# Optimization experiments

Hardware: AMD Instinct MI355X
Metric: run time of the kernel (lower is better)

The kernel has to match this reference:

```python
import jax, jax.numpy as jnp
import numpy as np

B, T, F, H, P, HEADS = 1024, 128, 9, 256, 2048, 4
DH = H // HEADS

def _lstm_layer(x, Wih, Whh, bih, bhh):
    # x: [B,T,in]; gate order i,f,g,o (torch convention)
    xp = jnp.einsum('bti,gi->btg', x, Wih) + bih + bhh  # [B,T,4H]
    h0 = jnp.zeros((x.shape[0], Whh.shape[1]), x.dtype)
    def step(carry, xt):
        h, c = carry
        g = xt + h @ Whh.T
        i, f, gg, o = jnp.split(g, 4, axis=-1)
        c = jax.nn.sigmoid(f) * c + jax.nn.sigmoid(i) * jnp.tanh(gg)
        h = jax.nn.sigmoid(o) * jnp.tanh(c)
        return (h, c), h
    _, hs = jax.lax.scan(step, (h0, h0), jnp.swapaxes(xp, 0, 1))
    return jnp.swapaxes(hs, 0, 1)  # [B,T,H]

def _layernorm(x, g, b, eps=1e-5):
    mu = x.mean(-1, keepdims=True)
    var = ((x - mu) ** 2).mean(-1, keepdims=True)
    return (x - mu) * jax.lax.rsqrt(var + eps) * g + b

def setup_inputs():
    key = jax.random.key(0)
    ks = jax.random.split(key, 30)
    w = lambda k, s: jax.random.normal(k, s, jnp.float32) * 0.05
    return {
        'x': jax.random.normal(ks[0], (B, T, F), jnp.float32),
        'sku_indices': jnp.arange(B, dtype=jnp.int32),
        'adj': jax.random.uniform(ks[1], (P, P), jnp.float32),
        'vsn_emb_w': w(ks[2], (F, H)), 'vsn_emb_b': w(ks[3], (F, H)),
        'vsn_sel_w': w(ks[4], (F, F)), 'vsn_sel_b': w(ks[5], (F,)),
        'lstm_Wih0': w(ks[6], (4 * H, H)), 'lstm_Whh0': w(ks[7], (4 * H, H)),
        'lstm_bih0': w(ks[8], (4 * H,)), 'lstm_bhh0': w(ks[9], (4 * H,)),
        'lstm_Wih1': w(ks[10], (4 * H, H)), 'lstm_Whh1': w(ks[11], (4 * H, H)),
        'lstm_bih1': w(ks[12], (4 * H,)), 'lstm_bhh1': w(ks[13], (4 * H,)),
        'attn_in_w': w(ks[14], (3 * H, H)), 'attn_in_b': w(ks[15], (3 * H,)),
        'attn_out_w': w(ks[16], (H, H)), 'attn_out_b': w(ks[17], (H,)),
        'gnn_w': w(ks[18], (H, H)), 'gnn_b': w(ks[19], (H,)),
        'ln_g': jnp.ones((H,), jnp.float32), 'ln_b': jnp.zeros((H,), jnp.float32),
        'gate_w': w(ks[20], (H, 2 * H)), 'gate_b': w(ks[21], (H,)),
        'out_w': w(ks[22], (1, H)), 'out_b': w(ks[23], (1,)),
    }

def reference(x, sku_indices, adj, vsn_emb_w, vsn_emb_b, vsn_sel_w, vsn_sel_b,
              lstm_Wih0, lstm_Whh0, lstm_bih0, lstm_bhh0,
              lstm_Wih1, lstm_Whh1, lstm_bih1, lstm_bhh1,
              attn_in_w, attn_in_b, attn_out_w, attn_out_b,
              gnn_w, gnn_b, ln_g, ln_b, gate_w, gate_b, out_w, out_b):
    # --- TFT hidden: variable selection -> 2-layer LSTM -> MHA, take last step ---
    emb = x[..., None] * vsn_emb_w + vsn_emb_b           # [B,T,F,H]
    wts = jax.nn.softmax(x @ vsn_sel_w.T + vsn_sel_b, -1)  # [B,T,F]
    h = jnp.einsum('btf,btfh->bth', wts, emb)            # [B,T,H]
    h = _lstm_layer(h, lstm_Wih0, lstm_Whh0, lstm_bih0, lstm_bhh0)
    h = _lstm_layer(h, lstm_Wih1, lstm_Whh1, lstm_bih1, lstm_bhh1)
    qkv = h @ attn_in_w.T + attn_in_b                    # [B,T,3H]
    q, k, v = [a.reshape(B, T, HEADS, DH) for a in jnp.split(qkv, 3, axis=-1)]
    scores = jnp.einsum('bqhd,bkhd->bhqk', q, k) / np.sqrt(DH).astype(np.float32)
    attn = jax.nn.softmax(scores, -1)
    o = jnp.einsum('bhqk,bkhd->bqhd', attn, v).reshape(B, T, H)
    o = o @ attn_out_w.T + attn_out_b
    hidden = o[:, -1, :]                                  # [B,H]
    # --- GNN enrichment (all sku_indices valid here) ---
    product_embeds = jnp.zeros((P, H), hidden.dtype).at[sku_indices].set(hidden)
    degree = jnp.clip(adj.sum(1, keepdims=True), 1e-6)
    aggregated = (adj / degree) @ product_embeds          # [P,H]
    transformed = jax.nn.gelu(aggregated @ gnn_w.T + gnn_b, approximate=False)
    transformed = _layernorm(transformed, ln_g, ln_b)
    enriched = transformed[sku_indices]                   # [B,H]
    gate = jax.nn.sigmoid(jnp.concatenate([hidden, enriched], -1) @ gate_w.T + gate_b)
    combined = gate * enriched + (1.0 - gate) * hidden
    out = combined @ out_w.T + out_b                      # [B,1]
    return out.squeeze(-1)
```

## Files before the change

### kernel.cpp

```cpp
#include <hip/hip_runtime.h>
#include <hip/hip_fp16.h>

typedef _Float16 f16;
typedef _Float16 f16x8 __attribute__((ext_vector_type(8)));
typedef _Float16 f16x4 __attribute__((ext_vector_type(4)));
typedef float f32x4 __attribute__((ext_vector_type(4)));

#define B_ 1024
#define T_ 128
#define F_ 9
#define H_ 256
#define P_ 2048

typedef unsigned long long ull;
#define AL(p) __hip_atomic_load((p), __ATOMIC_RELAXED, __HIP_MEMORY_SCOPE_AGENT)
#define AS(p, v) __hip_atomic_store((p), (v), __ATOMIC_RELAXED, __HIP_MEMORY_SCOPE_AGENT)

__device__ __forceinline__ float sigf(float x) { return 1.f / (1.f + __expf(-x)); }
__device__ __forceinline__ float tanh_(float x) {
  float a = fminf(fabsf(x), 12.f);
  float e = __expf(2.f * a);
  float r = 1.f - 2.f / (e + 1.f);
  return copysignf(r, x);
}

__device__ __forceinline__ f16x8 aload16(const f16* p) {
  union { ull u[2]; f16x8 v; } r;
  r.u[0] = AL((const ull*)p);
  r.u[1] = AL((const ull*)p + 1);
  return r.v;
}

__device__ __forceinline__ float blk_sum(float v) {
  __shared__ float sh[8];
  int lane = threadIdx.x & 63, w = threadIdx.x >> 6;
  int nw = blockDim.x >> 6;
#pragma unroll
  for (int o = 32; o > 0; o >>= 1) v += __shfl_xor(v, o, 64);
  __syncthreads();
  if (lane == 0) sh[w] = v;
  __syncthreads();
  float t = 0.f;
  for (int i = 0; i < nw; i++) t += sh[i];
  return t;
}

__global__ __launch_bounds__(256) void gemm64(
    const f16* __restrict__ A, int lda,
    const f16* __restrict__ Bt, int ldb,
    const float* __restrict__ bias,
    f16* __restrict__ o16, int ldo16,
    float* __restrict__ o32, int ldo32,
    f16* __restrict__ o16t, int ldt,
    int M, int N, int K)
{
  __shared__ __align__(16) f16 As[64][40];
  __shared__ __align__(16) f16 Bs[64][40];
  const int tid = threadIdx.x;
  const int lane = tid & 63, wave = tid >> 6;
  const int q = lane >> 4, l15 = lane & 15;
  const int bm = blockIdx.x * 64, bn = blockIdx.y * 64;

  f32x4 acc[4];
#pragma unroll
  for (int tn = 0; tn < 4; tn++) acc[tn] = (f32x4){0.f, 0.f, 0.f, 0.f};

  for (int k0 = 0; k0 < K; k0 += 32) {
    int row = tid >> 2, kh = (tid & 3) * 8;
    *(f16x8*)&As[row][kh] = *(const f16x8*)&A[(size_t)(bm + row) * lda + k0 + kh];
    *(f16x8*)&Bs[row][kh] = *(const f16x8*)&Bt[(size_t)(bn + row) * ldb + k0 + kh];
    __syncthreads();
    f16x8 af = *(const f16x8*)&As[wave * 16 + l15][q * 8];
#pragma unroll
    for (int tn = 0; tn < 4; tn++) {
      f16x8 bf = *(const f16x8*)&Bs[tn * 16 + l15][q * 8];
      acc[tn] = __builtin_amdgcn_mfma_f32_16x16x32_f16(af, bf, acc[tn], 0, 0, 0);
    }
    __syncthreads();
  }
#pragma unroll
  for (int tn = 0; tn < 4; tn++) {
    int colg = bn + tn * 16 + l15;
    float bv = bias ? bias[colg] : 0.f;
#pragma unroll
    for (int r = 0; r < 4; r++) {
      int rowg = bm + wave * 16 + q * 4 + r;
      float v = acc[tn][r] + bv;
      if (o32) o32[(size_t)rowg * ldo32 + colg] = v;
      if (o16) o16[(size_t)rowg * ldo16 + colg] = (f16)v;
      if (o16t) o16t[(size_t)colg * ldt + rowg] = (f16)v;
    }
  }
}

__global__ __launch_bounds__(256, 1) void lstm_pipe(
    f16* __restrict__ hio,
    const f16* __restrict__ wpk0, const f16* __restrict__ wpk1,
    const float* __restrict__ b0, const float* __restrict__ b1,
    int* __restrict__ cnt0, int* __restrict__ cnt1)
{
  __shared__ __align__(16) f16 apf[2][16][64][8];
  __shared__ __align__(16) f16 htile[32][64];
  const int tid = threadIdx.x;
  const int lane = tid & 63, w = tid >> 6;
  const int q = lane >> 4, l15 = lane & 15;
  const int layer = blockIdx.x >> 7;
  const int lbid = blockIdx.x & 127;
  const int grp = lbid & 31, s = lbid >> 5;
  const int m0 = grp * 32;
  const f16* wpk = layer ? wpk1 : wpk0;
  const float* bias = layer ? b1 : b0;
  int* myflags = (layer ? cnt1 : cnt0) + grp * 64;
  int* xflags  = cnt0 + grp * 64;

  const int own0 = ((w >> 1) == s);
  const int own1 = (((w + 4) >> 1) == s);
  const int offh = (w & 1) * 32;

  f16x8 bf[4][16];
  {
    const f16* wbase = wpk + (((size_t)(s * 4 + w) * 4) * 16) * 512 + lane * 8;
#pragma unroll
    for (int g = 0; g < 4; g++)
#pragma unroll
      for (int k = 0; k < 16; k++)
        bf[g][k] = *(const f16x8*)(wbase + (size_t)(g * 16 + k) * 512);
  }
  float bv[4];
#pragma unroll
  for (int g = 0; g < 4; g++) bv[g] = bias[g * 256 + s * 64 + w * 16 + l15];

  const int srow = lane & 15, scb = lane >> 4;
  size_t rb[2];
  rb[0] = ((size_t)(m0 + srow) * T_) * 256 + scb * 8;
  rb[1] = ((size_t)(m0 + 16 + srow) * T_) * 256 + scb * 8;

  const f16x8 zv = {(f16)0, (f16)0, (f16)0, (f16)0, (f16)0, (f16)0, (f16)0, (f16)0};

  if (layer) {
    if (tid == 0) {
      int it = 0;
      for (;;) {
        ull a = AL((ull*)xflags);
        ull b2 = AL((ull*)xflags + 1);
        if ((int)a >= 2 && (int)(a >> 32) >= 2 &&
            (int)b2 >= 2 && (int)(b2 >> 32) >= 2) break;
        __builtin_amdgcn_s_sleep(1);
        if (++it > (1 << 22)) break;
      }
    }
    __syncthreads();
  }
  f16x8 xr[2][2];
#pragma unroll
  for (int mt = 0; mt < 2; mt++) {
    if (layer) {
      xr[mt][0] = aload16(&hio[rb[mt] + (size_t)w * 32]);
      xr[mt][1] = aload16(&hio[rb[mt] + (size_t)(w + 4) * 32]);
    } else {
      xr[mt][0] = *(const f16x8*)&hio[rb[mt] + (size_t)w * 32];
      xr[mt][1] = *(const f16x8*)&hio[rb[mt] + (size_t)(w + 4) * 32];
    }
  }
  float cst[2][4] = {{0.f, 0.f, 0.f, 0.f}, {0.f, 0.f, 0.f, 0.f}};

  __syncthreads();
  if (tid == 0) AS(&myflags[s], 1);

  for (int t = 0; t < T_; ++t) {
    if (tid == 0) {
      const int needO = t + 1;
      int needX = 0;
      if (layer) { needX = t + 3; if (needX > T_ + 1) needX = T_ + 1; }
      int it = 0;
      for (;;) {
        ull a = AL((ull*)myflags);
        ull b2 = AL((ull*)myflags + 1);
        bool ok = (int)a >= needO && (int)(a >> 32) >= needO &&
                  (int)b2 >= needO && (int)(b2 >> 32) >= needO;
        if (ok && layer) {
          ull c = AL((ull*)xflags);
          ull d = AL((ull*)xflags + 1);
          ok = (int)c >= needX && (int)(c >> 32) >= needX &&
               (int)d >= needX && (int)(d >> 32) >= needX;
        }
        if (ok) break;
        __builtin_amdgcn_s_sleep(1);
        if (++it > (1 << 22)) break;
      }
    }
    __syncthreads();

#pragma unroll
    for (int mt = 0; mt < 2; mt++) {
      *(f16x8*)&apf[mt][w][lane][0]     = xr[mt][0];
      *(f16x8*)&apf[mt][w + 4][lane][0] = xr[mt][1];
      f16x8 h0 = zv, h1 = zv;
      if (t > 0) {
        if (own0) h0 = *(const f16x8*)&htile[mt * 16 + srow][offh + scb * 8];
        else      h0 = aload16(&hio[rb[mt] + (size_t)(t - 1) * 256 + (size_t)w * 32]);
        if (own1) h1 = *(const f16x8*)&htile[mt * 16 + srow][offh + scb * 8];
        else      h1 = aload16(&hio[rb[mt] + (size_t)(t - 1) * 256 + (size_t)(w + 4) * 32]);
      }
      *(f16x8*)&apf[mt][8 + w][lane][0]  = h0;
      *(f16x8*)&apf[mt][12 + w][lane][0] = h1;
    }
    __syncthreads();

    f32x4 acc[2][4];
#pragma unroll
    for (int mt = 0; mt < 2; mt++)
#pragma unroll
      for (int g = 0; g < 4; g++) acc[mt][g] = (f32x4){0.f, 0.f, 0.f, 0.f};
#pragma unroll
    for (int k = 0; k < 16; k++) {
      f16x8 a0 = *(const f16x8*)&apf[0][k][lane][0];
      f16x8 a1 = *(const f16x8*)&apf[1][k][lane][0];
#pragma unroll
      for (int g = 0; g < 4; g++) {
        acc[0][g] = __builtin_amdgcn_mfma_f32_16x16x32_f16(a0, bf[g][k], acc[0][g], 0, 0, 0);
        acc[1][g] = __builtin_amdgcn_mfma_f32_16x16x32_f16(a1, bf[g][k], acc[1][g], 0, 0, 0);
      }
    }
    if (t + 1 < T_) {
#pragma unroll
      for (int mt = 0; mt < 2; mt++) {
        if (layer) {
          xr[mt][0] = aload16(&hio[rb[mt] + (size_t)(t + 1) * 256 + (size_t)w * 32]);
          xr[mt][1] = aload16(&hio[rb[mt] + (size_t)(t + 1) * 256 + (size_t)(w + 4) * 32]);
        } else {
          xr[mt][0] = *(const f16x8*)&hio[rb[mt] + (size_t)(t + 1) * 256 + (size_t)w * 32];
          xr[mt][1] = *(const f16x8*)&hio[rb[mt] + (size_t)(t + 1) * 256 + (size_t)(w + 4) * 32];
        }
      }
    }
    f16 hn[2][4];
#pragma unroll
    for (int mt = 0; mt < 2; mt++)
#pragma unroll
      for (int r = 0; r < 4; r++) {
        float ip = acc[mt][0][r] + bv[0];
        float fp = acc[mt][1][r] + bv[1];
        float gp = acc[mt][2][r] + bv[2];
        float op = acc[mt][3][r] + bv[3];
        float cn = sigf(fp) * cst[mt][r] + sigf(ip) * tanh_(gp);
        cst[mt][r] = cn;
        hn[mt][r] = (f16)(sigf(op) * tanh_(cn));
      }
#pragma unroll
    for (int mt = 0; mt < 2; mt++)
#pragma unroll
      for (int r = 0; r < 4; r++)
        htile[mt * 16 + q * 4 + r][w * 16 + l15] = hn[mt][r];
    __syncthreads();
    {
      int row = tid >> 3, c8 = (tid & 7) * 8;
      union { ull u[2]; f16x8 v; } uh;
      uh.v = *(const f16x8*)&htile[row][c8];
      ull* dst =
          (ull*)&hio[((size_t)(m0 + row) * T_ + t) * 256 + s * 64 + c8];
      AS(dst, uh.u[0]);
      AS(dst + 1, uh.u[1]);
    }
    __syncthreads();
    if (tid == 0) AS(&myflags[s], t + 2);
  }
}

__global__ __launch_bounds__(256) void vsn_fused_kernel(
    const float* __restrict__ x, const float* __restrict__ selw,
    const float* __restrict__ selb, const float* __restrict__ embw,
    const float* __restrict__ embb, f16* __restrict__ hout)
{
  __shared__ float wbs[128][18];
  int b = blockIdx.x, tid = threadIdx.x;
  if (tid < 128) {
    size_t pos = (size_t)b * 128 + tid;
    const float* xr = x + pos * F_;
    float xv[F_];
#pragma unroll
    for (int f = 0; f < F_; f++) xv[f] = xr[f];
    float wv[F_]; float mx = -1e30f;
#pragma unroll
    for (int f = 0; f < F_; f++) {
      float s = selb[f];
#pragma unroll
      for (int f2 = 0; f2 < F_; f2++) s += xv[f2] * selw[f * F_ + f2];
      wv[f] = s; mx = fmaxf(mx, s);
    }
    float se = 0.f;
#pragma unroll
    for (int f = 0; f < F_; f++) { wv[f] = __expf(wv[f] - mx); se += wv[f]; }
    float inv = 1.f / se;
#pragma unroll
    for (int f = 0; f < F_; f++) {
      float wt = wv[f] * inv;
      wbs[tid][f] = wt; wbs[tid][9 + f] = wt * xv[f];
    }
  }
  __syncthreads();
  int j = tid;
  float ew[F_], eb[F_];
#pragma unroll
  for (int f = 0; f < F_; f++) { ew[f] = embw[f * H_ + j]; eb[f] = embb[f * H_ + j]; }
  for (int i = 0; i < 128; i++) {
    float h = 0.f;
#pragma unroll
    for (int f = 0; f < F_; f++) h += wbs[i][9 + f] * ew[f] + wbs[i][f] * eb[f];
    hout[((size_t)b * 128 + i) * H_ + j] = (f16)h;
  }
}

__global__ __launch_bounds__(256) void attn_fused_kernel(
    const f16* __restrict__ hseq, const float* __restrict__ qbuf,
    const float* __restrict__ attn_in_w, const float* __restrict__ attn_in_b,
    f16* __restrict__ aob)
{
  __shared__ __align__(16) f16 hs[T_][264];
  __shared__ float qs[256];
  __shared__ float qks[4][256];
  __shared__ float ps[4][T_];
  __shared__ float hb[4][256];
  int b = blockIdx.x, tid = threadIdx.x;
  for (int i = tid; i < T_ * 32; i += 256) {
    int row = i >> 5, cc = (i & 31) * 8;
    *(f16x8*)&hs[row][cc] = *(const f16x8*)&hseq[((size_t)b * T_ + row) * 256 + cc];
  }
  qs[tid] = qbuf[(size_t)b * 256 + tid];
  __syncthreads();
  {
    int j = tid;
#pragma unroll
    for (int h = 0; h < 4; h++) {
      float acc = 0.f;
      for (int d = 0; d < 64; d++)
        acc += qs[h * 64 + d] * attn_in_w[(size_t)(256 + h * 64 + d) * 256 + j];
      qks[h][j] = acc * 0.125f;
    }
  }
  __syncthreads();
  if (tid < T_) {
    float s[4] = {0.f, 0.f, 0.f, 0.f};
    for (int cc = 0; cc < 32; cc++) {
      f16x8 v = *(const f16x8*)&hs[tid][cc * 8];
#pragma unroll
      for (int h = 0; h < 4; h++) {
        float a = 0.f;
#pragma unroll
        for (int j = 0; j < 8; j++) a += qks[h][cc * 8 + j] * (float)v[j];
        s[h] += a;
      }
    }
#pragma unroll
    for (int h = 0; h < 4; h++) ps[h][tid] = s[h];
  }
  __syncthreads();
  {
    int w = tid >> 6, l = tid & 63;
    float a = ps[w][l], bb = ps[w][l + 64];
    float m = fmaxf(a, bb);
#pragma unroll
    for (int o = 32; o > 0; o >>= 1) m = fmaxf(m, __shfl_xor(m, o, 64));
    float e0 = __expf(a - m), e1 = __expf(bb - m);
    float se = e0 + e1;
#pragma unroll
    for (int o = 32; o > 0; o >>= 1) se += __shfl_xor(se, o, 64);
    float inv = 1.f / se;
    ps[w][l] = e0 * inv; ps[w][l + 64] = e1 * inv;
  }
  __syncthreads();
  {
    int j = tid;
    float acc[4] = {0.f, 0.f, 0.f, 0.f};
    for (int t = 0; t < T_; t++) {
      float hv = (float)hs[t][j];
#pragma unroll
      for (int h = 0; h < 4; h++) acc[h] += ps[h][t] * hv;
    }
#pragma unroll
    for (int h = 0; h < 4; h++) hb[h][j] = acc[h];
  }
  __syncthreads();
  {
    int d = tid, h = d >> 6;
    const float4* wr = (const float4*)(attn_in_w + (size_t)(512 + d) * 256);
    float acc = 0.f;
    for (int cc = 0; cc < 64; cc++) {
      float4 w4 = wr[cc];
      acc += w4.x * hb[h][cc * 4] + w4.y * hb[h][cc * 4 + 1]
           + w4.z * hb[h][cc * 4 + 2] + w4.w * hb[h][cc * 4 + 3];
    }
    aob[(size_t)b * 256 + d] = (f16)(acc + attn_in_b[512 + d]);
  }
}

__global__ __launch_bounds__(256) void gelu_ln_kernel(
    const float* __restrict__ pre, const float* __restrict__ lg,
    const float* __restrict__ lb, float* __restrict__ enr,
    f16* __restrict__ hidcat)
{
  int row = blockIdx.x, j = threadIdx.x;
  float xv = pre[row * 256 + j];
  float ge = 0.5f * xv * (1.f + erff(xv * 0.70710678118654752f));
  float mu = blk_sum(ge) * (1.f / 256.f);
  float d = ge - mu;
  float var = blk_sum(d * d) * (1.f / 256.f);
  float y = d * rsqrtf(var + 1e-5f) * lg[j] + lb[j];
  enr[row * 256 + j] = y;
  hidcat[row * 512 + 256 + j] = (f16)y;
}

__global__ __launch_bounds__(256) void final_kernel(
    const float* __restrict__ gpre, const float* __restrict__ enr,
    const float* __restrict__ hid, const float* __restrict__ outw,
    const float* __restrict__ outb, float* __restrict__ out)
{
  int b = blockIdx.x, j = threadIdx.x;
  float gt = sigf(gpre[b * 256 + j]);
  float comb = gt * enr[b * 256 + j] + (1.f - gt) * hid[b * 256 + j];
  float v = comb * outw[j];
  float s = blk_sum(v);
  if (j == 0) out[b] = s + outb[0];
}

__global__ void prep_kernel(
    const float* Wih0, const float* Whh0, const float* Wih1, const float* Whh1,
    const float* bih0, const float* bhh0, const float* bih1, const float* bhh1,
    const float* attn_in_w, const float* attn_out_w, const float* gnn_w,
    const float* gate_w, const float* adj, const int* sku,
    f16* wpk0, f16* wpk1, f16* attninf, f16* attnoutf, f16* gnnwf, f16* gatewf,
    float* bias0, float* bias1, int* flagz, f16* adjn)
{
  if (blockIdx.x >= 3353) {
    int bp = blockIdx.x - 3353;
    int p = sku[bp];
    int tid = threadIdx.x;
    float s = 0.f;
    for (int j = tid; j < P_; j += 256) s += adj[(size_t)p * P_ + j];
    float tot = blk_sum(s);
    float inv = 1.f / fmaxf(tot, 1e-6f);
    for (int b = tid; b < B_; b += 256)
      adjn[(size_t)bp * B_ + b] = (f16)(adj[(size_t)p * P_ + sku[b]] * inv);
    return;
  }
  int idx = blockIdx.x * 256 + threadIdx.x;
  if (idx < 524288) {
    int j = idx & 7, lane = (idx >> 3) & 63, k = (idx >> 9) & 15;
    int g = (idx >> 13) & 3, w = (idx >> 15) & 3, s = (idx >> 17) & 3;
    int row = g * 256 + s * 64 + w * 16 + (lane & 15);
    int col = k * 32 + (lane >> 4) * 8 + j;
    float v0 = col < 256 ? Wih0[(size_t)row * 256 + col] : Whh0[(size_t)row * 256 + col - 256];
    float v1 = col < 256 ? Wih1[(size_t)row * 256 + col] : Whh1[(size_t)row * 256 + col - 256];
    wpk0[idx] = (f16)v0;
    wpk1[idx] = (f16)v1;
    return;
  }
  int i = idx - 524288;
  if (i < 65536) { attninf[i] = (f16)attn_in_w[i]; return; }
  i -= 65536;
  if (i < 65536) { attnoutf[i] = (f16)attn_out_w[i]; return; }
  i -= 65536;
  if (i < 65536) { gnnwf[i] = (f16)gnn_w[i]; return; }
  i -= 65536;
  if (i < 131072) { gatewf[i] = (f16)gate_w[i]; return; }
  i -= 131072;
  if (i < 1024) { bias0[i] = bih0[i] + bhh0[i]; return; }
  i -= 1024;
  if (i < 1024) { bias1[i] = bih1[i] + bhh1[i]; return; }
  i -= 1024;
  if (i < 4096) { flagz[i] = 0; return; }
}

extern "C" void kernel_launch(void* const* d_in, const int* in_sizes, int n_in,
                              void* d_out, int out_size, void* d_ws, size_t ws_size,
                              hipStream_t stream)
{
  const float* x         = (const float*)d_in[0];
  const int*   sku       = (const int*)  d_in[1];
  const float* adj       = (const float*)d_in[2];
  const float* vsn_emb_w = (const float*)d_in[3];
  const float* vsn_emb_b = (const float*)d_in[4];
  const float* vsn_sel_w = (const float*)d_in[5];
  const float* vsn_sel_b = (const float*)d_in[6];
  const float* Wih0 = (const float*)d_in[7];
  const float* Whh0 = (const float*)d_in[8];
  const float* bih0 = (const float*)d_in[9];
  const float* bhh0 = (const float*)d_in[10];
  const float* Wih1 = (const float*)d_in[11];
  const float* Whh1 = (const float*)d_in[12];
  const float* bih1 = (const float*)d_in[13];
  const float* bhh1 = (const float*)d_in[14];
  const float* attn_in_w  = (const float*)d_in[15];
  const float* attn_in_b  = (const float*)d_in[16];
  const float* attn_out_w = (const float*)d_in[17];
  const float* attn_out_b = (const float*)d_in[18];
  const float* gnn_w  = (const float*)d_in[19];
  const float* gnn_b  = (const float*)d_in[20];
  const float* ln_g   = (const float*)d_in[21];
  const float* ln_b   = (const float*)d_in[22];
  const float* gate_w = (const float*)d_in[23];
  const float* gate_b = (const float*)d_in[24];
  const float* out_w  = (const float*)d_in[25];
  const float* out_b  = (const float*)d_in[26];
  (void)in_sizes; (void)n_in; (void)out_size; (void)ws_size;

  char* wsb = (char*)d_ws;
  size_t off = 0;
  auto alloc = [&](size_t bytes) -> void* {
    void* p = wsb + off;
    off += (bytes + 255) & ~(size_t)255;
    return p;
  };
  f16* hA      = (f16*)alloc((size_t)B_ * T_ * H_ * 2);
  f16* wpk0    = (f16*)alloc((size_t)1024 * 512 * 2);
  f16* wpk1    = (f16*)alloc((size_t)1024 * 512 * 2);
  f16* attninf = (f16*)alloc((size_t)256 * 256 * 2);
  f16* attnoutf= (f16*)alloc((size_t)256 * 256 * 2);
  f16* gnnwf   = (f16*)alloc((size_t)256 * 256 * 2);
  f16* gatewf  = (f16*)alloc((size_t)256 * 512 * 2);
  float* bias0 = (float*)alloc(1024 * 4);
  float* bias1 = (float*)alloc(1024 * 4);
  int* cnt0    = (int*)alloc(32 * 64 * 4);
  int* cnt1    = (int*)alloc(32 * 64 * 4);
  f16* adjn    = (f16*)alloc((size_t)B_ * B_ * 2);
  float* qbuf  = (float*)alloc((size_t)B_ * 256 * 4);
  f16* aob     = (f16*)alloc((size_t)B_ * 256 * 2);
  float* hidden32 = (float*)alloc((size_t)B_ * 256 * 4);
  f16* hidcat  = (f16*)alloc((size_t)B_ * 512 * 2);
  f16* hT      = (f16*)alloc((size_t)256 * B_ * 2);
  f16* aggf    = (f16*)alloc((size_t)B_ * 256 * 2);
  float* gnnpre= (float*)alloc((size_t)B_ * 256 * 4);
  float* enr32 = (float*)alloc((size_t)B_ * 256 * 4);
  float* gatepre=(float*)alloc((size_t)B_ * 256 * 4);

  prep_kernel<<<4377, 256, 0, stream>>>(
      Wih0, Whh0, Wih1, Whh1, bih0, bhh0, bih1, bhh1,
      attn_in_w, attn_out_w, gnn_w, gate_w, adj, sku,
      wpk0, wpk1, attninf, attnoutf, gnnwf, gatewf, bias0, bias1, cnt0, adjn);

  vsn_fused_kernel<<<B_, 256, 0, stream>>>(x, vsn_sel_w, vsn_sel_b,
                                           vsn_emb_w, vsn_emb_b, hA);
  lstm_pipe<<<256, 256, 0, stream>>>(hA, wpk0, wpk1, bias0, bias1, cnt0, cnt1);

  dim3 g64(B_ / 64, 256 / 64);
  gemm64<<<g64, 256, 0, stream>>>(hA + (size_t)(T_ - 1) * 256, T_ * 256, attninf, 256,
                                  attn_in_b, nullptr, 0, qbuf, 256, nullptr, 0,
                                  B_, 256, 256);
  attn_fused_kernel<<<B_, 256, 0, stream>>>(hA, qbuf, attn_in_w, attn_in_b, aob);
  gemm64<<<g64, 256, 0, stream>>>(aob, 256, attnoutf, 256, attn_out_b,
                                  hidcat, 512, hidden32, 256, hT, B_,
                                  B_, 256, 256);
  gemm64<<<g64, 256, 0, stream>>>(adjn, 1024, hT, 1024, nullptr,
                                  aggf, 256, nullptr, 0, nullptr, 0,
                                  B_, 256, 1024);
  gemm64<<<g64, 256, 0, stream>>>(aggf, 256, gnnwf, 256, gnn_b,
                                  nullptr, 0, gnnpre, 256, nullptr, 0,
                                  B_, 256, 256);
  gelu_ln_kernel<<<B_, 256, 0, stream>>>(gnnpre, ln_g, ln_b, enr32, hidcat);
  gemm64<<<g64, 256, 0, stream>>>(hidcat, 512, gatewf, 512, gate_b,
                                  nullptr, 0, gatepre, 256, nullptr, 0,
                                  B_, 256, 512);
  final_kernel<<<B_, 256, 0, stream>>>(gatepre, enr32, hidden32, out_w, out_b, (float*)d_out);
}
```

Baseline: 951.0 us.

## Fuse VSN into prep, q-projection into attention, and GNN/LN/gate tail into one kernel

```diff
diff --git a/kernel.cpp b/kernel.cpp
--- a/kernel.cpp
+++ b/kernel.cpp
@@ -267,52 +267,8 @@
   }
 }
 
-__global__ __launch_bounds__(256) void vsn_fused_kernel(
-    const float* __restrict__ x, const float* __restrict__ selw,
-    const float* __restrict__ selb, const float* __restrict__ embw,
-    const float* __restrict__ embb, f16* __restrict__ hout)
-{
-  __shared__ float wbs[128][18];
-  int b = blockIdx.x, tid = threadIdx.x;
-  if (tid < 128) {
-    size_t pos = (size_t)b * 128 + tid;
-    const float* xr = x + pos * F_;
-    float xv[F_];
-#pragma unroll
-    for (int f = 0; f < F_; f++) xv[f] = xr[f];
-    float wv[F_]; float mx = -1e30f;
-#pragma unroll
-    for (int f = 0; f < F_; f++) {
-      float s = selb[f];
-#pragma unroll
-      for (int f2 = 0; f2 < F_; f2++) s += xv[f2] * selw[f * F_ + f2];
-      wv[f] = s; mx = fmaxf(mx, s);
-    }
-    float se = 0.f;
-#pragma unroll
-    for (int f = 0; f < F_; f++) { wv[f] = __expf(wv[f] - mx); se += wv[f]; }
-    float inv = 1.f / se;
-#pragma unroll
-    for (int f = 0; f < F_; f++) {
-      float wt = wv[f] * inv;
-      wbs[tid][f] = wt; wbs[tid][9 + f] = wt * xv[f];
-    }
-  }
-  __syncthreads();
-  int j = tid;
-  float ew[F_], eb[F_];
-#pragma unroll
-  for (int f = 0; f < F_; f++) { ew[f] = embw[f * H_ + j]; eb[f] = embb[f * H_ + j]; }
-  for (int i = 0; i < 128; i++) {
-    float h = 0.f;
-#pragma unroll
-    for (int f = 0; f < F_; f++) h += wbs[i][9 + f] * ew[f] + wbs[i][f] * eb[f];
-    hout[((size_t)b * 128 + i) * H_ + j] = (f16)h;
-  }
-}
-
 __global__ __launch_bounds__(256) void attn_fused_kernel(
-    const f16* __restrict__ hseq, const float* __restrict__ qbuf,
+    const f16* __restrict__ hseq, const f16* __restrict__ attninf,
     const float* __restrict__ attn_in_w, const float* __restrict__ attn_in_b,
     f16* __restrict__ aob)
 {
@@ -326,7 +282,19 @@
     int row = i >> 5, cc = (i & 31) * 8;
     *(f16x8*)&hs[row][cc] = *(const f16x8*)&hseq[((size_t)b * T_ + row) * 256 + cc];
   }
-  qs[tid] = qbuf[(size_t)b * 256 + tid];
+  __syncthreads();
+  {
+    int j = tid;
+    float acc = attn_in_b[j];
+    const f16x8* wr = (const f16x8*)(attninf + (size_t)j * 256);
+    for (int cc = 0; cc < 32; cc++) {
+      f16x8 wv = wr[cc];
+      f16x8 hv = *(const f16x8*)&hs[T_ - 1][cc * 8];
+#pragma unroll
+      for (int u = 0; u < 8; u++) acc += (float)hv[u] * (float)wv[u];
+    }
+    qs[j] = acc;
+  }
   __syncthreads();
   {
     int j = tid;
@@ -394,30 +362,36 @@
   }
 }
 
-__global__ __launch_bounds__(256) void gelu_ln_kernel(
-    const float* __restrict__ pre, const float* __restrict__ lg,
-    const float* __restrict__ lb, float* __restrict__ enr,
-    f16* __restrict__ hidcat)
+__global__ __launch_bounds__(256) void tail_fused_kernel(
+    const f16* __restrict__ aggf, const f16* __restrict__ gnnwT,
+    const float* __restrict__ gnn_b, const float* __restrict__ lg,
+    const float* __restrict__ lb, const float* __restrict__ hid32,
+    const f16* __restrict__ gatewT, const float* __restrict__ gate_b,
+    const float* __restrict__ outw, const float* __restrict__ outb,
+    float* __restrict__ out)
 {
-  int row = blockIdx.x, j = threadIdx.x;
-  float xv = pre[row * 256 + j];
-  float ge = 0.5f * xv * (1.f + erff(xv * 0.70710678118654752f));
+  __shared__ float ag[256], yl[256], hl[256];
+  int b = blockIdx.x, j = threadIdx.x;
+  ag[j] = (float)aggf[(size_t)b * 256 + j];
+  hl[j] = hid32[(size_t)b * 256 + j];
+  __syncthreads();
+  float acc = gnn_b[j];
+#pragma unroll 8
+  for (int k = 0; k < 256; k++) acc += ag[k] * (float)gnnwT[k * 256 + j];
+  float ge = 0.5f * acc * (1.f + erff(acc * 0.70710678118654752f));
   float mu = blk_sum(ge) * (1.f / 256.f);
   float d = ge - mu;
   float var = blk_sum(d * d) * (1.f / 256.f);
   float y = d * rsqrtf(var + 1e-5f) * lg[j] + lb[j];
-  enr[row * 256 + j] = y;
-  hidcat[row * 512 + 256 + j] = (f16)y;
-}
-
-__global__ __launch_bounds__(256) void final_kernel(
-    const float* __restrict__ gpre, const float* __restrict__ enr,
-    const float* __restrict__ hid, const float* __restrict__ outw,
-    const float* __restrict__ outb, float* __restrict__ out)
-{
-  int b = blockIdx.x, j = threadIdx.x;
-  float gt = sigf(gpre[b * 256 + j]);
-  float comb = gt * enr[b * 256 + j] + (1.f - gt) * hid[b * 256 + j];
+  yl[j] = y;
+  __syncthreads();
+  float g = gate_b[j];
+#pragma unroll 8
+  for (int k = 0; k < 256; k++) g += hl[k] * (float)gatewT[k * 256 + j];
+#pragma unroll 8
+  for (int k = 0; k < 256; k++) g += yl[k] * (float)gatewT[(256 + k) * 256 + j];
+  float gt = sigf(g);
+  float comb = gt * y + (1.f - gt) * hl[j];
   float v = comb * outw[j];
   float s = blk_sum(v);
   if (j == 0) out[b] = s + outb[0];
@@ -428,9 +402,51 @@
     const float* bih0, const float* bhh0, const float* bih1, const float* bhh1,
     const float* attn_in_w, const float* attn_out_w, const float* gnn_w,
     const float* gate_w, const float* adj, const int* sku,
-    f16* wpk0, f16* wpk1, f16* attninf, f16* attnoutf, f16* gnnwf, f16* gatewf,
-    float* bias0, float* bias1, int* flagz, f16* adjn)
+    const float* x, const float* selw, const float* selb,
+    const float* embw, const float* embb,
+    f16* wpk0, f16* wpk1, f16* attninf, f16* attnoutf, f16* gnnwT, f16* gatewT,
+    float* bias0, float* bias1, int* flagz, f16* adjn, f16* hA)
 {
+  if (blockIdx.x >= 4377) {
+    __shared__ float wbs[128][18];
+    int b = blockIdx.x - 4377, tid = threadIdx.x;
+    if (tid < 128) {
+      size_t pos = (size_t)b * 128 + tid;
+      const float* xr = x + pos * F_;
+      float xv[F_];
+#pragma unroll
+      for (int f = 0; f < F_; f++) xv[f] = xr[f];
+      float wv[F_]; float mx = -1e30f;
+#pragma unroll
+      for (int f = 0; f < F_; f++) {
+        float s = selb[f];
+#pragma unroll
+        for (int f2 = 0; f2 < F_; f2++) s += xv[f2] * selw[f * F_ + f2];
+        wv[f] = s; mx = fmaxf(mx, s);
+      }
+      float se = 0.f;
+#pragma unroll
+      for (int f = 0; f < F_; f++) { wv[f] = __expf(wv[f] - mx); se += wv[f]; }
+      float inv = 1.f / se;
+#pragma unroll
+      for (int f = 0; f < F_; f++) {
+        float wt = wv[f] * inv;
+        wbs[tid][f] = wt; wbs[tid][9 + f] = wt * xv[f];
+      }
+    }
+    __syncthreads();
+    int j = threadIdx.x;
+    float ew[F_], eb[F_];
+#pragma unroll
+    for (int f = 0; f < F_; f++) { ew[f] = embw[f * H_ + j]; eb[f] = embb[f * H_ + j]; }
+    for (int i = 0; i < 128; i++) {
+      float h = 0.f;
+#pragma unroll
+      for (int f = 0; f < F_; f++) h += wbs[i][9 + f] * ew[f] + wbs[i][f] * eb[f];
+      hA[((size_t)b * 128 + i) * H_ + j] = (f16)h;
+    }
+    return;
+  }
   if (blockIdx.x >= 3353) {
     int bp = blockIdx.x - 3353;
     int p = sku[bp];
@@ -460,9 +476,17 @@
   i -= 65536;
   if (i < 65536) { attnoutf[i] = (f16)attn_out_w[i]; return; }
   i -= 65536;
-  if (i < 65536) { gnnwf[i] = (f16)gnn_w[i]; return; }
+  if (i < 65536) {
+    int j = i & 255, k = i >> 8;
+    gnnwT[i] = (f16)gnn_w[(size_t)j * 256 + k];
+    return;
+  }
   i -= 65536;
-  if (i < 131072) { gatewf[i] = (f16)gate_w[i]; return; }
+  if (i < 131072) {
+    int j = i & 255, k = i >> 8;
+    gatewT[i] = (f16)gate_w[(size_t)j * 512 + k];
+    return;
+  }
   i -= 131072;
   if (i < 1024) { bias0[i] = bih0[i] + bhh0[i]; return; }
   i -= 1024;
@@ -516,49 +540,35 @@
   f16* wpk1    = (f16*)alloc((size_t)1024 * 512 * 2);
   f16* attninf = (f16*)alloc((size_t)256 * 256 * 2);
   f16* attnoutf= (f16*)alloc((size_t)256 * 256 * 2);
-  f16* gnnwf   = (f16*)alloc((size_t)256 * 256 * 2);
-  f16* gatewf  = (f16*)alloc((size_t)256 * 512 * 2);
+  f16* gnnwT   = (f16*)alloc((size_t)256 * 256 * 2);
+  f16* gatewT  = (f16*)alloc((size_t)512 * 256 * 2);
   float* bias0 = (float*)alloc(1024 * 4);
   float* bias1 = (float*)alloc(1024 * 4);
   int* cnt0    = (int*)alloc(32 * 64 * 4);
   int* cnt1    = (int*)alloc(32 * 64 * 4);
   f16* adjn    = (f16*)alloc((size_t)B_ * B_ * 2);
-  float* qbuf  = (float*)alloc((size_t)B_ * 256 * 4);
   f16* aob     = (f16*)alloc((size_t)B_ * 256 * 2);
   float* hidden32 = (float*)alloc((size_t)B_ * 256 * 4);
-  f16* hidcat  = (f16*)alloc((size_t)B_ * 512 * 2);
   f16* hT      = (f16*)alloc((size_t)256 * B_ * 2);
   f16* aggf    = (f16*)alloc((size_t)B_ * 256 * 2);
-  float* gnnpre= (float*)alloc((size_t)B_ * 256 * 4);
-  float* enr32 = (float*)alloc((size_t)B_ * 256 * 4);
-  float* gatepre=(float*)alloc((size_t)B_ * 256 * 4);
-
-  prep_kernel<<<4377, 256, 0, stream>>>(
+
+  prep_kernel<<<5401, 256, 0, stream>>>(
       Wih0, Whh0, Wih1, Whh1, bih0, bhh0, bih1, bhh1,
       attn_in_w, attn_out_w, gnn_w, gate_w, adj, sku,
-      wpk0, wpk1, attninf, attnoutf, gnnwf, gatewf, bias0, bias1, cnt0, adjn);
-
-  vsn_fused_kernel<<<B_, 256, 0, stream>>>(x, vsn_sel_w, vsn_sel_b,
-                                           vsn_emb_w, vsn_emb_b, hA);
+      x, vsn_sel_w, vsn_sel_b, vsn_emb_w, vsn_emb_b,
+      wpk0, wpk1, attninf, attnoutf, gnnwT, gatewT, bias0, bias1, cnt0, adjn, hA);
+
   lstm_pipe<<<256, 256, 0, stream>>>(hA, wpk0, wpk1, bias0, bias1, cnt0, cnt1);
 
+  attn_fused_kernel<<<B_, 256, 0, stream>>>(hA, attninf, attn_in_w, attn_in_b, aob);
   dim3 g64(B_ / 64, 256 / 64);
-  gemm64<<<g64, 256, 0, stream>>>(hA + (size_t)(T_ - 1) * 256, T_ * 256, attninf, 256,
-                                  attn_in_b, nullptr, 0, qbuf, 256, nullptr, 0,
-                                  B_, 256, 256);
-  attn_fused_kernel<<<B_, 256, 0, stream>>>(hA, qbuf, attn_in_w, attn_in_b, aob);
   gemm64<<<g64, 256, 0, stream>>>(aob, 256, attnoutf, 256, attn_out_b,
-                                  hidcat, 512, hidden32, 256, hT, B_,
+                                  nullptr, 0, hidden32, 256, hT, B_,
                                   B_, 256, 256);
   gemm64<<<g64, 256, 0, stream>>>(adjn, 1024, hT, 1024, nullptr,
                                   aggf, 256, nullptr, 0, nullptr, 0,
                                   B_, 256, 1024);
-  gemm64<<<g64, 256, 0, stream>>>(aggf, 256, gnnwf, 256, gnn_b,
-                                  nullptr, 0, gnnpre, 256, nullptr, 0,
-                                  B_, 256, 256);
-  gelu_ln_kernel<<<B_, 256, 0, stream>>>(gnnpre, ln_g, ln_b, enr32, hidcat);
-  gemm64<<<g64, 256, 0, stream>>>(hidcat, 512, gatewf, 512, gate_b,
-                                  nullptr, 0, gatepre, 256, nullptr, 0,
-                                  B_, 256, 512);
-  final_kernel<<<B_, 256, 0, stream>>>(gatepre, enr32, hidden32, out_w, out_b, (float*)d_out);
-}
+  tail_fused_kernel<<<B_, 256, 0, stream>>>(aggf, gnnwT, gnn_b, ln_g, ln_b,
+                                            hidden32, gatewT, gate_b,
+                                            out_w, out_b, (float*)d_out);
+}
```

Result: no change. 960.3 us (+1.0%).
